# Kernel optimization log

Measured on AMD Instinct MI355X. Metric: run time of the kernel, lower is better.

The kernel has to match this reference:

```python
import jax, jax.numpy as jnp
import numpy as np

B, S, CS, H, G, P, N = 2, 4096, 256, 32, 1, 64, 128
NC = S // CS  # number of chunks


def setup_inputs() -> dict:
    key = jax.random.key(0)
    ks = jax.random.split(key, 7)
    cb = jax.random.normal(ks[0], (B, NC, G, CS, CS), jnp.float32) * 0.1
    x = jax.random.normal(ks[1], (B, S, H, P), jnp.float32)
    dt = jax.random.uniform(ks[2], (B, H, NC, CS), jnp.float32, 0.0, 0.1)
    # dA_cumsum is a (negative) cumulative log-decay within each chunk
    dA_cumsum = -jnp.cumsum(jax.random.uniform(ks[3], (B, H, NC, CS), jnp.float32, 0.0, 0.05), axis=-1)
    C = jax.random.normal(ks[4], (B, S, G, N), jnp.float32) * 0.1
    prev_states = jax.random.normal(ks[5], (B, NC, H, P, N), jnp.float32) * 0.1
    D = jax.random.normal(ks[6], (H,), jnp.float32)
    return {"cb": cb, "x": x, "dt": dt, "dA_cumsum": dA_cumsum, "C": C,
            "prev_states": prev_states, "D": D}


def reference(cb, x, dt, dA_cumsum, C, prev_states, D):
    # Reshape sequence into chunks
    x_c = x.reshape(B, NC, CS, H, P)          # b c l h p
    C_c = C.reshape(B, NC, CS, G, N)          # b c l g n
    rep = H // G
    # expand groups to heads
    C_h = jnp.repeat(C_c, rep, axis=3)        # b c l h n
    cb_h = jnp.repeat(cb, rep, axis=2)        # b c h m k

    # --- inter-chunk contribution: (C @ prev_states^T) * exp(dA_cs_m) ---
    out_inter = jnp.einsum('bclhn,bchpn->bclhp', C_h, prev_states)
    scale_m = jnp.exp(dA_cumsum)              # b h c l
    out_inter = out_inter * scale_m.transpose(0, 2, 3, 1)[..., None]

    # --- intra-chunk causal contribution ---
    # decay[m,k] = exp(dA_m - dA_k), masked to m >= k, weighted by dt_k
    dA = dA_cumsum                            # b h c l
    decay = jnp.exp(dA[..., :, None] - dA[..., None, :])  # b h c m k
    causal = jnp.tril(jnp.ones((CS, CS), jnp.bool_))
    scores = jnp.where(causal, cb_h.transpose(0, 2, 1, 3, 4) * decay * dt[..., None, :], 0.0)  # b h c m k
    out_intra = jnp.einsum('bhcmk,bckhp->bcmhp', scores, x_c)

    out = out_inter + out_intra + x_c * D[None, None, None, :, None]
    return out.reshape(B, S, H, P)
```

## Files before the change

kernel.cpp:

```cpp
#include <hip/hip_runtime.h>


typedef unsigned short u16;
typedef __bf16 v8bf __attribute__((ext_vector_type(8)));
typedef unsigned short v8u16 __attribute__((ext_vector_type(8)));
typedef float v4f __attribute__((ext_vector_type(4)));

#define LDB 264

__device__ __forceinline__ unsigned pk2f(float a, float b) {
  u16 x = __builtin_bit_cast(u16, (__bf16)a);
  u16 y = __builtin_bit_cast(u16, (__bf16)b);
  return (unsigned)x | ((unsigned)y << 16);
}
__device__ __forceinline__ v8bf cvt8(float4 lo, float4 hi) {
  v8bf r;
  r[0] = (__bf16)lo.x; r[1] = (__bf16)lo.y; r[2] = (__bf16)lo.z; r[3] = (__bf16)lo.w;
  r[4] = (__bf16)hi.x; r[5] = (__bf16)hi.y; r[6] = (__bf16)hi.z; r[7] = (__bf16)hi.w;
  return r;
}
__device__ __forceinline__ v8bf cvt8_mask(float4 lo, float4 hi, int k0, int m) {
  const float av[8] = {lo.x, lo.y, lo.z, lo.w, hi.x, hi.y, hi.z, hi.w};
  v8bf r;
#pragma unroll
  for (int j = 0; j < 8; j++) r[j] = (__bf16)((k0 + j <= m) ? av[j] : 0.f);
  return r;
}

__global__ __launch_bounds__(512, 4) void mamba_cs_kernel(
    const float* __restrict__ cbp,
    const float* __restrict__ xp,
    const float* __restrict__ dtp,
    const float* __restrict__ dAp,
    const float* __restrict__ Cp,
    const float* __restrict__ pvp,
    const float* __restrict__ Dp,
    float* __restrict__ outp)
{
  __shared__ u16 sB[64 * LDB];

  const int bid0 = blockIdx.x;
  const int wg = ((bid0 & 7) << 7) | (bid0 >> 3);
  const int h = wg & 31;
  const int c = (wg >> 5) & 15;
  const int b = wg >> 9;
  const int t = threadIdx.x;
  const int lane = t & 63;
  const int wid = t >> 6;
  const int row = lane & 15;
  const int q = lane >> 4;
  const int qo = q * 8;

  const int Ta = wid;
  const int Tb = 15 - wid;
  const int ma = Ta * 16 + row;
  const int mb = Tb * 16 + row;

  const int base_hc = ((b * 32 + h) * 16 + c) * 256;
  const float Dh = Dp[h];

  const float* CBbase = cbp + (size_t)(b * 16 + c) * 65536;
  const float* Cbase  = Cp + (size_t)(b * 4096 + c * 256) * 128;
  const float* Pbase  = pvp + (size_t)((b * 16 + c) * 32 + h) * 8192;
  const float* Xbase  = xp + ((size_t)(b * 4096 + c * 256) * 32 + h) * 64;

  v4f acc[2][4];
  float4 dAq[2];

#pragma unroll
  for (int tt = 0; tt < 2; ++tt) {
    const int T = tt ? Tb : Ta;
    const int m4 = T * 16 + q * 4;
    const float4 dA4 = *(const float4*)(dAp + base_hc + m4);
    const float4 dt4 = *(const float4*)(dtp + base_hc + m4);
    dAq[tt] = dA4;
    float xv[4][4];
#pragma unroll
    for (int r = 0; r < 4; ++r) {
      const float* xr = Xbase + (size_t)(m4 + r) * 2048 + row;
#pragma unroll
      for (int pt = 0; pt < 4; ++pt) xv[r][pt] = xr[pt * 16];
    }
    const float dv[4] = {dA4.x, dA4.y, dA4.z, dA4.w};
    const float tv[4] = {dt4.x, dt4.y, dt4.z, dt4.w};
    float wi[4], w[4];
#pragma unroll
    for (int r = 0; r < 4; ++r) {
      wi[r] = __expf(-dv[r]);
      w[r] = wi[r] * tv[r];
    }
#pragma unroll
    for (int pt = 0; pt < 4; ++pt) {
      v4f a;
#pragma unroll
      for (int r = 0; r < 4; ++r) a[r] = Dh * xv[r][pt] * wi[r];
      acc[tt][pt] = a;
      u16* srow = &sB[(pt * 16 + row) * LDB + m4];
      *(unsigned*)(srow)     = pk2f(w[0] * xv[0][pt], w[1] * xv[1][pt]);
      *(unsigned*)(srow + 2) = pk2f(w[2] * xv[2][pt], w[3] * xv[3][pt]);
    }
  }

  {
    const float* Cra = Cbase + (size_t)ma * 128;
    const float* Crb = Cbase + (size_t)mb * 128;
#pragma unroll
    for (int kf = 0; kf < 4; ++kf) {
      const int no = kf * 32 + qo;
      v8bf bf[4];
#pragma unroll
      for (int pt = 0; pt < 4; ++pt) {
        const float* pr = Pbase + (size_t)(pt * 16 + row) * 128 + no;
        bf[pt] = cvt8(*(const float4*)pr, *(const float4*)(pr + 4));
      }
      const v8bf a0 = cvt8(*(const float4*)(Cra + no), *(const float4*)(Cra + no + 4));
      const v8bf a1 = cvt8(*(const float4*)(Crb + no), *(const float4*)(Crb + no + 4));
#pragma unroll
      for (int pt = 0; pt < 4; ++pt) {
        acc[0][pt] = __builtin_amdgcn_mfma_f32_16x16x32_bf16(a0, bf[pt], acc[0][pt], 0, 0, 0);
        acc[1][pt] = __builtin_amdgcn_mfma_f32_16x16x32_bf16(a1, bf[pt], acc[1][pt], 0, 0, 0);
      }
    }
  }

  __syncthreads();

  {
    const float* cba = CBbase + (size_t)ma * 256;
    const float* cbb = CBbase + (size_t)mb * 256;
    const int kfa = Ta >> 1;
    const int kfb = Tb >> 1;
    float4 alo = *(const float4*)(cba + qo);
    float4 ahi = *(const float4*)(cba + qo + 4);
    float4 blo = *(const float4*)(cbb + qo);
    float4 bhi = *(const float4*)(cbb + qo + 4);
    for (int kf = 0; kf <= kfb; ++kf) {
      const int ko = kf * 32 + qo;
      float4 nalo = alo, nahi = ahi, nblo = blo, nbhi = bhi;
      if (kf < kfb) {
        const int nko = ko + 32;
        nblo = *(const float4*)(cbb + nko);
        nbhi = *(const float4*)(cbb + nko + 4);
        if (kf + 1 <= kfa) {
          nalo = *(const float4*)(cba + nko);
          nahi = *(const float4*)(cba + nko + 4);
        }
      }
      v8bf bf[4];
#pragma unroll
      for (int pt = 0; pt < 4; ++pt)
        bf[pt] = __builtin_bit_cast(v8bf, *(const v8u16*)&sB[(pt * 16 + row) * LDB + ko]);
      {
        const v8bf ab = (kf == kfb) ? cvt8_mask(blo, bhi, ko, mb) : cvt8(blo, bhi);
#pragma unroll
        for (int pt = 0; pt < 4; ++pt)
          acc[1][pt] = __builtin_amdgcn_mfma_f32_16x16x32_bf16(ab, bf[pt], acc[1][pt], 0, 0, 0);
      }
      if (kf <= kfa) {
        const v8bf aa = (kf == kfa) ? cvt8_mask(alo, ahi, ko, ma) : cvt8(alo, ahi);
#pragma unroll
        for (int pt = 0; pt < 4; ++pt)
          acc[0][pt] = __builtin_amdgcn_mfma_f32_16x16x32_bf16(aa, bf[pt], acc[0][pt], 0, 0, 0);
      }
      alo = nalo; ahi = nahi; blo = nblo; bhi = nbhi;
    }
  }

  float* Obase = outp + ((size_t)(b * 4096 + c * 256) * 32 + h) * 64;
  const int Ts[2] = {Ta, Tb};
#pragma unroll
  for (int tt = 0; tt < 2; ++tt) {
    const int mBase = Ts[tt] * 16 + q * 4;
    const float ev[4] = {dAq[tt].x, dAq[tt].y, dAq[tt].z, dAq[tt].w};
#pragma unroll
    for (int r = 0; r < 4; ++r) {
      const float e = __expf(ev[r]);
      float* orow = Obase + (size_t)(mBase + r) * 2048 + row;
#pragma unroll
      for (int pt = 0; pt < 4; ++pt) orow[pt * 16] = acc[tt][pt][r] * e;
    }
  }
}

extern "C" void kernel_launch(void* const* d_in, const int* in_sizes, int n_in,
                              void* d_out, int out_size, void* d_ws, size_t ws_size,
                              hipStream_t stream) {
  const float* cb = (const float*)d_in[0];
  const float* x = (const float*)d_in[1];
  const float* dt = (const float*)d_in[2];
  const float* dA = (const float*)d_in[3];
  const float* C = (const float*)d_in[4];
  const float* pv = (const float*)d_in[5];
  const float* D = (const float*)d_in[6];
  float* out = (float*)d_out;
  mamba_cs_kernel<<<dim3(1024), dim3(512), 0, stream>>>(cb, x, dt, dA, C, pv, D, out);
}
```

Before: 213.4 us.

## Stage prev_states through LDS as bf16 and prefetch C/CB loads

Loads the per-head prev_states tile once cooperatively with coalesced float4 reads, converts it to bf16 and stores it in a new shared buffer. Previously each wave re-read it from global memory with strided per-lane loads. All x/dA/dt loads are issued before any compute, and the C and CB first fragments are prefetched before the barrier, with C software-pipelined across the inter-chunk MFMA loop. The cost is extra LDS (about 17KB more per block) and more live registers, which may reduce occupancy under the 512x4 launch bounds.

```diff
diff --git a/kernel.cpp b/kernel.cpp
--- a/kernel.cpp
+++ b/kernel.cpp
@@ -7,6 +7,7 @@
 typedef float v4f __attribute__((ext_vector_type(4)));
 
 #define LDB 264
+#define LDP 136
 
 __device__ __forceinline__ unsigned pk2f(float a, float b) {
   u16 x = __builtin_bit_cast(u16, (__bf16)a);
@@ -38,6 +39,7 @@
     float* __restrict__ outp)
 {
   __shared__ u16 sB[64 * LDB];
+  __shared__ u16 sP[64 * LDP];
 
   const int bid0 = blockIdx.x;
   const int wg = ((bid0 & 7) << 7) | (bid0 >> 3);
@@ -64,76 +66,111 @@
   const float* Pbase  = pvp + (size_t)((b * 16 + c) * 32 + h) * 8192;
   const float* Xbase  = xp + ((size_t)(b * 4096 + c * 256) * 32 + h) * 64;
 
+  float4 pf[4];
+  {
+    const float4* Pv = (const float4*)Pbase;
+#pragma unroll
+    for (int i = 0; i < 4; i++) pf[i] = Pv[i * 512 + t];
+  }
+
   v4f acc[2][4];
   float4 dAq[2];
 
-#pragma unroll
-  for (int tt = 0; tt < 2; ++tt) {
-    const int T = tt ? Tb : Ta;
-    const int m4 = T * 16 + q * 4;
-    const float4 dA4 = *(const float4*)(dAp + base_hc + m4);
-    const float4 dt4 = *(const float4*)(dtp + base_hc + m4);
-    dAq[tt] = dA4;
-    float xv[4][4];
-#pragma unroll
-    for (int r = 0; r < 4; ++r) {
-      const float* xr = Xbase + (size_t)(m4 + r) * 2048 + row;
-#pragma unroll
-      for (int pt = 0; pt < 4; ++pt) xv[r][pt] = xr[pt * 16];
-    }
-    const float dv[4] = {dA4.x, dA4.y, dA4.z, dA4.w};
-    const float tv[4] = {dt4.x, dt4.y, dt4.z, dt4.w};
-    float wi[4], w[4];
-#pragma unroll
-    for (int r = 0; r < 4; ++r) {
-      wi[r] = __expf(-dv[r]);
-      w[r] = wi[r] * tv[r];
-    }
+  {
+    float4 dA4[2], dt4[2];
+    float xv[2][4][4];
+#pragma unroll
+    for (int tt = 0; tt < 2; ++tt) {
+      const int T = tt ? Tb : Ta;
+      const int m4 = T * 16 + q * 4;
+      dA4[tt] = *(const float4*)(dAp + base_hc + m4);
+      dt4[tt] = *(const float4*)(dtp + base_hc + m4);
+#pragma unroll
+      for (int r = 0; r < 4; ++r) {
+        const float* xr = Xbase + (size_t)(m4 + r) * 2048 + row;
+#pragma unroll
+        for (int pt = 0; pt < 4; ++pt) xv[tt][r][pt] = xr[pt * 16];
+      }
+    }
+#pragma unroll
+    for (int tt = 0; tt < 2; ++tt) {
+      const int T = tt ? Tb : Ta;
+      const int m4 = T * 16 + q * 4;
+      dAq[tt] = dA4[tt];
+      const float dv[4] = {dA4[tt].x, dA4[tt].y, dA4[tt].z, dA4[tt].w};
+      const float tv[4] = {dt4[tt].x, dt4[tt].y, dt4[tt].z, dt4[tt].w};
+      float wi[4], w[4];
+#pragma unroll
+      for (int r = 0; r < 4; ++r) {
+        wi[r] = __expf(-dv[r]);
+        w[r] = wi[r] * tv[r];
+      }
+#pragma unroll
+      for (int pt = 0; pt < 4; ++pt) {
+        v4f a;
+#pragma unroll
+        for (int r = 0; r < 4; ++r) a[r] = Dh * xv[tt][r][pt] * wi[r];
+        acc[tt][pt] = a;
+        u16* srow = &sB[(pt * 16 + row) * LDB + m4];
+        *(unsigned*)(srow)     = pk2f(w[0] * xv[tt][0][pt], w[1] * xv[tt][1][pt]);
+        *(unsigned*)(srow + 2) = pk2f(w[2] * xv[tt][2][pt], w[3] * xv[tt][3][pt]);
+      }
+    }
+  }
+
+#pragma unroll
+  for (int i = 0; i < 4; i++) {
+    const int idx = i * 512 + t;
+    const int prow = idx >> 5;
+    const int c4 = idx & 31;
+    u16* s = &sP[prow * LDP + c4 * 4];
+    *(unsigned*)(s)     = pk2f(pf[i].x, pf[i].y);
+    *(unsigned*)(s + 2) = pk2f(pf[i].z, pf[i].w);
+  }
+
+  const float* Cra = Cbase + (size_t)ma * 128;
+  const float* Crb = Cbase + (size_t)mb * 128;
+  const float* cba = CBbase + (size_t)ma * 256;
+  const float* cbb = CBbase + (size_t)mb * 256;
+  float4 ca0 = *(const float4*)(Cra + qo);
+  float4 ca1 = *(const float4*)(Cra + qo + 4);
+  float4 cc0 = *(const float4*)(Crb + qo);
+  float4 cc1 = *(const float4*)(Crb + qo + 4);
+  float4 alo = *(const float4*)(cba + qo);
+  float4 ahi = *(const float4*)(cba + qo + 4);
+  float4 blo = *(const float4*)(cbb + qo);
+  float4 bhi = *(const float4*)(cbb + qo + 4);
+
+  __syncthreads();
+
+#pragma unroll
+  for (int kf = 0; kf < 4; ++kf) {
+    const int no = kf * 32 + qo;
+    float4 nca0 = ca0, nca1 = ca1, ncc0 = cc0, ncc1 = cc1;
+    if (kf < 3) {
+      const int nn = no + 32;
+      nca0 = *(const float4*)(Cra + nn);
+      nca1 = *(const float4*)(Cra + nn + 4);
+      ncc0 = *(const float4*)(Crb + nn);
+      ncc1 = *(const float4*)(Crb + nn + 4);
+    }
+    v8bf bf[4];
+#pragma unroll
+    for (int pt = 0; pt < 4; ++pt)
+      bf[pt] = __builtin_bit_cast(v8bf, *(const v8u16*)&sP[(pt * 16 + row) * LDP + no]);
+    const v8bf a0 = cvt8(ca0, ca1);
+    const v8bf a1 = cvt8(cc0, cc1);
 #pragma unroll
     for (int pt = 0; pt < 4; ++pt) {
-      v4f a;
-#pragma unroll
-      for (int r = 0; r < 4; ++r) a[r] = Dh * xv[r][pt] * wi[r];
-      acc[tt][pt] = a;
-      u16* srow = &sB[(pt * 16 + row) * LDB + m4];
-      *(unsigned*)(srow)     = pk2f(w[0] * xv[0][pt], w[1] * xv[1][pt]);
-      *(unsigned*)(srow + 2) = pk2f(w[2] * xv[2][pt], w[3] * xv[3][pt]);
-    }
+      acc[0][pt] = __builtin_amdgcn_mfma_f32_16x16x32_bf16(a0, bf[pt], acc[0][pt], 0, 0, 0);
+      acc[1][pt] = __builtin_amdgcn_mfma_f32_16x16x32_bf16(a1, bf[pt], acc[1][pt], 0, 0, 0);
+    }
+    ca0 = nca0; ca1 = nca1; cc0 = ncc0; cc1 = ncc1;
   }
 
   {
-    const float* Cra = Cbase + (size_t)ma * 128;
-    const float* Crb = Cbase + (size_t)mb * 128;
-#pragma unroll
-    for (int kf = 0; kf < 4; ++kf) {
-      const int no = kf * 32 + qo;
-      v8bf bf[4];
-#pragma unroll
-      for (int pt = 0; pt < 4; ++pt) {
-        const float* pr = Pbase + (size_t)(pt * 16 + row) * 128 + no;
-        bf[pt] = cvt8(*(const float4*)pr, *(const float4*)(pr + 4));
-      }
-      const v8bf a0 = cvt8(*(const float4*)(Cra + no), *(const float4*)(Cra + no + 4));
-      const v8bf a1 = cvt8(*(const float4*)(Crb + no), *(const float4*)(Crb + no + 4));
-#pragma unroll
-      for (int pt = 0; pt < 4; ++pt) {
-        acc[0][pt] = __builtin_amdgcn_mfma_f32_16x16x32_bf16(a0, bf[pt], acc[0][pt], 0, 0, 0);
-        acc[1][pt] = __builtin_amdgcn_mfma_f32_16x16x32_bf16(a1, bf[pt], acc[1][pt], 0, 0, 0);
-      }
-    }
-  }
-
-  __syncthreads();
-
-  {
-    const float* cba = CBbase + (size_t)ma * 256;
-    const float* cbb = CBbase + (size_t)mb * 256;
     const int kfa = Ta >> 1;
     const int kfb = Tb >> 1;
-    float4 alo = *(const float4*)(cba + qo);
-    float4 ahi = *(const float4*)(cba + qo + 4);
-    float4 blo = *(const float4*)(cbb + qo);
-    float4 bhi = *(const float4*)(cbb + qo + 4);
     for (int kf = 0; kf <= kfb; ++kf) {
       const int ko = kf * 32 + qo;
       float4 nalo = alo, nahi = ahi, nblo = blo, nbhi = bhi;
```

Result: faster. 197.2 us (-7.6%).

## Process four heads per block, reusing C and CB fragments with register-prefetched stages

Applied to the files above, without the earlier changes.

Each block now handles four heads of one (batch, chunk) instead of one head, so the C and masked CB operand fragments are loaded and converted to bf16 once and kept in registers across heads. prev_states is staged through a new shared-memory tile, and the next head's x, dt, dA and prev_states are prefetched into registers while the current head's MFMAs run. This is meant to cut redundant global traffic on cb and C and hide load latency. In exchange the grid drops from 1024 to 256 blocks, which may underfill the GPU, and the higher register use lowers the occupancy bound.

```diff
diff --git a/kernel.cpp b/kernel.cpp
--- a/kernel.cpp
+++ b/kernel.cpp
@@ -7,6 +7,7 @@
 typedef float v4f __attribute__((ext_vector_type(4)));
 
 #define LDB 264
+#define LDP 136
 
 __device__ __forceinline__ unsigned pk2f(float a, float b) {
   u16 x = __builtin_bit_cast(u16, (__bf16)a);
@@ -27,7 +28,13 @@
   return r;
 }
 
-__global__ __launch_bounds__(512, 4) void mamba_cs_kernel(
+struct SR {
+  float4 pf[4];
+  float4 dA4[2], dt4[2];
+  float xv[2][4][4];
+};
+
+__global__ __launch_bounds__(512, 2) void mamba_cs_kernel(
     const float* __restrict__ cbp,
     const float* __restrict__ xp,
     const float* __restrict__ dtp,
@@ -38,12 +45,15 @@
     float* __restrict__ outp)
 {
   __shared__ u16 sB[64 * LDB];
+  __shared__ u16 sP[64 * LDP];
 
   const int bid0 = blockIdx.x;
-  const int wg = ((bid0 & 7) << 7) | (bid0 >> 3);
-  const int h = wg & 31;
-  const int c = (wg >> 5) & 15;
-  const int b = wg >> 9;
+  const int wg = ((bid0 & 7) << 5) | (bid0 >> 3);
+  const int hg = wg & 7;
+  const int c = (wg >> 3) & 15;
+  const int b = wg >> 7;
+  const int h0 = hg * 4;
+
   const int t = threadIdx.x;
   const int lane = t & 63;
   const int wid = t >> 6;
@@ -55,131 +65,178 @@
   const int Tb = 15 - wid;
   const int ma = Ta * 16 + row;
   const int mb = Tb * 16 + row;
-
-  const int base_hc = ((b * 32 + h) * 16 + c) * 256;
-  const float Dh = Dp[h];
+  const int kfa = Ta >> 1;
+  const int kfb = Tb >> 1;
 
   const float* CBbase = cbp + (size_t)(b * 16 + c) * 65536;
   const float* Cbase  = Cp + (size_t)(b * 4096 + c * 256) * 128;
-  const float* Pbase  = pvp + (size_t)((b * 16 + c) * 32 + h) * 8192;
-  const float* Xbase  = xp + ((size_t)(b * 4096 + c * 256) * 32 + h) * 64;
+
+  const float* Cra = Cbase + (size_t)ma * 128;
+  const float* Crb = Cbase + (size_t)mb * 128;
+  const float* cba = CBbase + (size_t)ma * 256;
+  const float* cbb = CBbase + (size_t)mb * 256;
+
+  v8bf Ca[4], Cb2[4];
+  v8bf Aa[4], Ab[8];
+#pragma unroll
+  for (int kf = 0; kf < 4; ++kf) {
+    const int no = kf * 32 + qo;
+    Ca[kf]  = cvt8(*(const float4*)(Cra + no), *(const float4*)(Cra + no + 4));
+    Cb2[kf] = cvt8(*(const float4*)(Crb + no), *(const float4*)(Crb + no + 4));
+  }
+#pragma unroll
+  for (int kf = 0; kf < 4; ++kf)
+    if (kf <= kfa) {
+      const int ko = kf * 32 + qo;
+      const float4 lo = *(const float4*)(cba + ko);
+      const float4 hi = *(const float4*)(cba + ko + 4);
+      Aa[kf] = (kf == kfa) ? cvt8_mask(lo, hi, ko, ma) : cvt8(lo, hi);
+    }
+#pragma unroll
+  for (int kf = 0; kf < 8; ++kf)
+    if (kf <= kfb) {
+      const int ko = kf * 32 + qo;
+      const float4 lo = *(const float4*)(cbb + ko);
+      const float4 hi = *(const float4*)(cbb + ko + 4);
+      Ab[kf] = (kf == kfb) ? cvt8_mask(lo, hi, ko, mb) : cvt8(lo, hi);
+    }
 
   v4f acc[2][4];
   float4 dAq[2];
 
-#pragma unroll
-  for (int tt = 0; tt < 2; ++tt) {
-    const int T = tt ? Tb : Ta;
-    const int m4 = T * 16 + q * 4;
-    const float4 dA4 = *(const float4*)(dAp + base_hc + m4);
-    const float4 dt4 = *(const float4*)(dtp + base_hc + m4);
-    dAq[tt] = dA4;
-    float xv[4][4];
-#pragma unroll
-    for (int r = 0; r < 4; ++r) {
-      const float* xr = Xbase + (size_t)(m4 + r) * 2048 + row;
-#pragma unroll
-      for (int pt = 0; pt < 4; ++pt) xv[r][pt] = xr[pt * 16];
-    }
-    const float dv[4] = {dA4.x, dA4.y, dA4.z, dA4.w};
-    const float tv[4] = {dt4.x, dt4.y, dt4.z, dt4.w};
-    float wi[4], w[4];
-#pragma unroll
-    for (int r = 0; r < 4; ++r) {
-      wi[r] = __expf(-dv[r]);
-      w[r] = wi[r] * tv[r];
-    }
-#pragma unroll
-    for (int pt = 0; pt < 4; ++pt) {
-      v4f a;
-#pragma unroll
-      for (int r = 0; r < 4; ++r) a[r] = Dh * xv[r][pt] * wi[r];
-      acc[tt][pt] = a;
-      u16* srow = &sB[(pt * 16 + row) * LDB + m4];
-      *(unsigned*)(srow)     = pk2f(w[0] * xv[0][pt], w[1] * xv[1][pt]);
-      *(unsigned*)(srow + 2) = pk2f(w[2] * xv[2][pt], w[3] * xv[3][pt]);
-    }
-  }
-
-  {
-    const float* Cra = Cbase + (size_t)ma * 128;
-    const float* Crb = Cbase + (size_t)mb * 128;
+  auto stage_load = [&](int h, SR& R) {
+    const float4* Pv = (const float4*)(pvp + (size_t)((b * 16 + c) * 32 + h) * 8192);
+#pragma unroll
+    for (int i = 0; i < 4; i++) R.pf[i] = Pv[i * 512 + t];
+    const int bhc = ((b * 32 + h) * 16 + c) * 256;
+    const float* Xb = xp + ((size_t)(b * 4096 + c * 256) * 32 + h) * 64;
+#pragma unroll
+    for (int tt = 0; tt < 2; ++tt) {
+      const int m4 = (tt ? Tb : Ta) * 16 + q * 4;
+      R.dA4[tt] = *(const float4*)(dAp + bhc + m4);
+      R.dt4[tt] = *(const float4*)(dtp + bhc + m4);
+#pragma unroll
+      for (int r = 0; r < 4; ++r) {
+        const float* xr = Xb + (size_t)(m4 + r) * 2048 + row;
+#pragma unroll
+        for (int pt = 0; pt < 4; ++pt) R.xv[tt][r][pt] = xr[pt * 16];
+      }
+    }
+  };
+
+  auto commit = [&](SR& R, float Dh) {
+#pragma unroll
+    for (int i = 0; i < 4; i++) {
+      const int idx = i * 512 + t, prow = idx >> 5, c4 = idx & 31;
+      u16* s = &sP[prow * LDP + c4 * 4];
+      *(unsigned*)(s)     = pk2f(R.pf[i].x, R.pf[i].y);
+      *(unsigned*)(s + 2) = pk2f(R.pf[i].z, R.pf[i].w);
+    }
+#pragma unroll
+    for (int tt = 0; tt < 2; ++tt) {
+      const int m4 = (tt ? Tb : Ta) * 16 + q * 4;
+      dAq[tt] = R.dA4[tt];
+      const float dv[4] = {R.dA4[tt].x, R.dA4[tt].y, R.dA4[tt].z, R.dA4[tt].w};
+      const float tv[4] = {R.dt4[tt].x, R.dt4[tt].y, R.dt4[tt].z, R.dt4[tt].w};
+      float wi[4], w[4];
+#pragma unroll
+      for (int r = 0; r < 4; ++r) {
+        wi[r] = __expf(-dv[r]);
+        w[r] = wi[r] * tv[r];
+      }
+#pragma unroll
+      for (int pt = 0; pt < 4; ++pt) {
+        v4f a;
+#pragma unroll
+        for (int r = 0; r < 4; ++r) a[r] = Dh * R.xv[tt][r][pt] * wi[r];
+        acc[tt][pt] = a;
+        u16* srow = &sB[(pt * 16 + row) * LDB + m4];
+        *(unsigned*)(srow)     = pk2f(w[0] * R.xv[tt][0][pt], w[1] * R.xv[tt][1][pt]);
+        *(unsigned*)(srow + 2) = pk2f(w[2] * R.xv[tt][2][pt], w[3] * R.xv[tt][3][pt]);
+      }
+    }
+  };
+
+  auto compute = [&]() {
 #pragma unroll
     for (int kf = 0; kf < 4; ++kf) {
       const int no = kf * 32 + qo;
       v8bf bf[4];
 #pragma unroll
+      for (int pt = 0; pt < 4; ++pt)
+        bf[pt] = __builtin_bit_cast(v8bf, *(const v8u16*)&sP[(pt * 16 + row) * LDP + no]);
+#pragma unroll
       for (int pt = 0; pt < 4; ++pt) {
-        const float* pr = Pbase + (size_t)(pt * 16 + row) * 128 + no;
-        bf[pt] = cvt8(*(const float4*)pr, *(const float4*)(pr + 4));
-      }
-      const v8bf a0 = cvt8(*(const float4*)(Cra + no), *(const float4*)(Cra + no + 4));
-      const v8bf a1 = cvt8(*(const float4*)(Crb + no), *(const float4*)(Crb + no + 4));
-#pragma unroll
-      for (int pt = 0; pt < 4; ++pt) {
-        acc[0][pt] = __builtin_amdgcn_mfma_f32_16x16x32_bf16(a0, bf[pt], acc[0][pt], 0, 0, 0);
-        acc[1][pt] = __builtin_amdgcn_mfma_f32_16x16x32_bf16(a1, bf[pt], acc[1][pt], 0, 0, 0);
-      }
-    }
-  }
-
-  __syncthreads();
-
-  {
-    const float* cba = CBbase + (size_t)ma * 256;
-    const float* cbb = CBbase + (size_t)mb * 256;
-    const int kfa = Ta >> 1;
-    const int kfb = Tb >> 1;
-    float4 alo = *(const float4*)(cba + qo);
-    float4 ahi = *(const float4*)(cba + qo + 4);
-    float4 blo = *(const float4*)(cbb + qo);
-    float4 bhi = *(const float4*)(cbb + qo + 4);
-    for (int kf = 0; kf <= kfb; ++kf) {
-      const int ko = kf * 32 + qo;
-      float4 nalo = alo, nahi = ahi, nblo = blo, nbhi = bhi;
-      if (kf < kfb) {
-        const int nko = ko + 32;
-        nblo = *(const float4*)(cbb + nko);
-        nbhi = *(const float4*)(cbb + nko + 4);
-        if (kf + 1 <= kfa) {
-          nalo = *(const float4*)(cba + nko);
-          nahi = *(const float4*)(cba + nko + 4);
+        acc[0][pt] = __builtin_amdgcn_mfma_f32_16x16x32_bf16(Ca[kf], bf[pt], acc[0][pt], 0, 0, 0);
+        acc[1][pt] = __builtin_amdgcn_mfma_f32_16x16x32_bf16(Cb2[kf], bf[pt], acc[1][pt], 0, 0, 0);
+      }
+    }
+#pragma unroll
+    for (int kf = 0; kf < 8; ++kf) {
+      if (kf <= kfb) {
+        const int ko = kf * 32 + qo;
+        v8bf bf[4];
+#pragma unroll
+        for (int pt = 0; pt < 4; ++pt)
+          bf[pt] = __builtin_bit_cast(v8bf, *(const v8u16*)&sB[(pt * 16 + row) * LDB + ko]);
+#pragma unroll
+        for (int pt = 0; pt < 4; ++pt)
+          acc[1][pt] = __builtin_amdgcn_mfma_f32_16x16x32_bf16(Ab[kf], bf[pt], acc[1][pt], 0, 0, 0);
+        if (kf <= kfa) {
+#pragma unroll
+          for (int pt = 0; pt < 4; ++pt)
+            acc[0][pt] = __builtin_amdgcn_mfma_f32_16x16x32_bf16(Aa[kf], bf[pt], acc[0][pt], 0, 0, 0);
         }
       }
-      v8bf bf[4];
-#pragma unroll
-      for (int pt = 0; pt < 4; ++pt)
-        bf[pt] = __builtin_bit_cast(v8bf, *(const v8u16*)&sB[(pt * 16 + row) * LDB + ko]);
-      {
-        const v8bf ab = (kf == kfb) ? cvt8_mask(blo, bhi, ko, mb) : cvt8(blo, bhi);
-#pragma unroll
-        for (int pt = 0; pt < 4; ++pt)
-          acc[1][pt] = __builtin_amdgcn_mfma_f32_16x16x32_bf16(ab, bf[pt], acc[1][pt], 0, 0, 0);
-      }
-      if (kf <= kfa) {
-        const v8bf aa = (kf == kfa) ? cvt8_mask(alo, ahi, ko, ma) : cvt8(alo, ahi);
-#pragma unroll
-        for (int pt = 0; pt < 4; ++pt)
-          acc[0][pt] = __builtin_amdgcn_mfma_f32_16x16x32_bf16(aa, bf[pt], acc[0][pt], 0, 0, 0);
-      }
-      alo = nalo; ahi = nahi; blo = nblo; bhi = nbhi;
-    }
-  }
-
-  float* Obase = outp + ((size_t)(b * 4096 + c * 256) * 32 + h) * 64;
-  const int Ts[2] = {Ta, Tb};
-#pragma unroll
-  for (int tt = 0; tt < 2; ++tt) {
-    const int mBase = Ts[tt] * 16 + q * 4;
-    const float ev[4] = {dAq[tt].x, dAq[tt].y, dAq[tt].z, dAq[tt].w};
-#pragma unroll
-    for (int r = 0; r < 4; ++r) {
-      const float e = __expf(ev[r]);
-      float* orow = Obase + (size_t)(mBase + r) * 2048 + row;
-#pragma unroll
-      for (int pt = 0; pt < 4; ++pt) orow[pt * 16] = acc[tt][pt][r] * e;
-    }
-  }
+    }
+  };
+
+  auto epilogue = [&](int h) {
+    float* Ob = outp + ((size_t)(b * 4096 + c * 256) * 32 + h) * 64;
+#pragma unroll
+    for (int tt = 0; tt < 2; ++tt) {
+      const int mBase = (tt ? Tb : Ta) * 16 + q * 4;
+      const float ev[4] = {dAq[tt].x, dAq[tt].y, dAq[tt].z, dAq[tt].w};
+#pragma unroll
+      for (int r = 0; r < 4; ++r) {
+        const float e = __expf(ev[r]);
+        float* orow = Ob + (size_t)(mBase + r) * 2048 + row;
+#pragma unroll
+        for (int pt = 0; pt < 4; ++pt) orow[pt * 16] = acc[tt][pt][r] * e;
+      }
+    }
+  };
+
+  const float D0 = Dp[h0], D1 = Dp[h0 + 1], D2 = Dp[h0 + 2], D3 = Dp[h0 + 3];
+
+  SR RA, RB;
+  stage_load(h0, RA);
+
+  commit(RA, D0);
+  __syncthreads();
+  stage_load(h0 + 1, RB);
+  compute();
+  epilogue(h0);
+  __syncthreads();
+
+  commit(RB, D1);
+  __syncthreads();
+  stage_load(h0 + 2, RA);
+  compute();
+  epilogue(h0 + 1);
+  __syncthreads();
+
+  commit(RA, D2);
+  __syncthreads();
+  stage_load(h0 + 3, RB);
+  compute();
+  epilogue(h0 + 2);
+  __syncthreads();
+
+  commit(RB, D3);
+  __syncthreads();
+  compute();
+  epilogue(h0 + 3);
 }
 
 extern "C" void kernel_launch(void* const* d_in, const int* in_sizes, int n_in,
@@ -193,5 +250,5 @@
   const float* pv = (const float*)d_in[5];
   const float* D = (const float*)d_in[6];
   float* out = (float*)d_out;
-  mamba_cs_kernel<<<dim3(1024), dim3(512), 0, stream>>>(cb, x, dt, dA, C, pv, D, out);
-}
+  mamba_cs_kernel<<<dim3(256), dim3(512), 0, stream>>>(cb, x, dt, dA, C, pv, D, out);
+}
```

Result: faster. 176.4 us (-17.4%).

## Process four heads per block with staged prev_states in LDS and prefetch

Applied to the files above, without the earlier changes.

Each block now covers four consecutive heads of one (batch, chunk) with 1024 threads, one 16-row tile per wave, instead of one head with 512 threads and paired tiles. The C operand is converted to bf16 once and kept in registers for all four heads. The next head's prev_states, x, dt and dA are prefetched while the current head computes, and prev_states is staged into LDS as bf16 instead of being read per lane from global. The grid shrinks to 256 blocks, which cuts parallelism, and the per-wave causal work is now uneven across waves instead of being balanced by tile pairing.

```diff
diff --git a/kernel.cpp b/kernel.cpp
--- a/kernel.cpp
+++ b/kernel.cpp
@@ -5,8 +5,10 @@
 typedef __bf16 v8bf __attribute__((ext_vector_type(8)));
 typedef unsigned short v8u16 __attribute__((ext_vector_type(8)));
 typedef float v4f __attribute__((ext_vector_type(4)));
+typedef unsigned v2u __attribute__((ext_vector_type(2)));
 
 #define LDB 264
+#define LDP 136
 
 __device__ __forceinline__ unsigned pk2f(float a, float b) {
   u16 x = __builtin_bit_cast(u16, (__bf16)a);
@@ -27,7 +29,7 @@
   return r;
 }
 
-__global__ __launch_bounds__(512, 4) void mamba_cs_kernel(
+__global__ __launch_bounds__(1024, 4) void mamba_cs_kernel(
     const float* __restrict__ cbp,
     const float* __restrict__ xp,
     const float* __restrict__ dtp,
@@ -38,12 +40,15 @@
     float* __restrict__ outp)
 {
   __shared__ u16 sB[64 * LDB];
+  __shared__ u16 sP[64 * LDP];
 
   const int bid0 = blockIdx.x;
-  const int wg = ((bid0 & 7) << 7) | (bid0 >> 3);
-  const int h = wg & 31;
-  const int c = (wg >> 5) & 15;
-  const int b = wg >> 9;
+  const int wg = ((bid0 & 7) << 5) | (bid0 >> 3);
+  const int hg = wg & 7;
+  const int c = (wg >> 3) & 15;
+  const int b = wg >> 7;
+  const int h0 = hg * 4;
+
   const int t = threadIdx.x;
   const int lane = t & 63;
   const int wid = t >> 6;
@@ -51,36 +56,57 @@
   const int q = lane >> 4;
   const int qo = q * 8;
 
-  const int Ta = wid;
-  const int Tb = 15 - wid;
-  const int ma = Ta * 16 + row;
-  const int mb = Tb * 16 + row;
-
-  const int base_hc = ((b * 32 + h) * 16 + c) * 256;
-  const float Dh = Dp[h];
+  const int T = wid;
+  const int ma = T * 16 + row;
+  const int m4 = T * 16 + q * 4;
+  const int kfa = T >> 1;
 
   const float* CBbase = cbp + (size_t)(b * 16 + c) * 65536;
-  const float* Cbase  = Cp + (size_t)(b * 4096 + c * 256) * 128;
-  const float* Pbase  = pvp + (size_t)((b * 16 + c) * 32 + h) * 8192;
-  const float* Xbase  = xp + ((size_t)(b * 4096 + c * 256) * 32 + h) * 64;
+  const float* cba = CBbase + (size_t)ma * 256;
+  const float* Cra = Cp + (size_t)(b * 4096 + c * 256) * 128 + (size_t)ma * 128;
 
-  v4f acc[2][4];
-  float4 dAq[2];
+  v8bf Ca[4];
+#pragma unroll
+  for (int kf = 0; kf < 4; ++kf) {
+    const int no = kf * 32 + qo;
+    Ca[kf] = cvt8(*(const float4*)(Cra + no), *(const float4*)(Cra + no + 4));
+  }
 
-#pragma unroll
-  for (int tt = 0; tt < 2; ++tt) {
-    const int T = tt ? Tb : Ta;
-    const int m4 = T * 16 + q * 4;
-    const float4 dA4 = *(const float4*)(dAp + base_hc + m4);
-    const float4 dt4 = *(const float4*)(dtp + base_hc + m4);
-    dAq[tt] = dA4;
-    float xv[4][4];
+  const float4 Dv = *(const float4*)(Dp + h0);
+  const float Dhs[4] = {Dv.x, Dv.y, Dv.z, Dv.w};
+
+  float4 pf0, pf1, dA4, dt4;
+  float xv[4][4];
+  v4f acc[4];
+  float4 dAq;
+
+  auto stage_load = [&](int h) {
+    const float4* Pv = (const float4*)(pvp + (size_t)((b * 16 + c) * 32 + h) * 8192);
+    pf0 = Pv[t];
+    pf1 = Pv[1024 + t];
+    const int bhc = ((b * 32 + h) * 16 + c) * 256;
+    dA4 = *(const float4*)(dAp + bhc + m4);
+    dt4 = *(const float4*)(dtp + bhc + m4);
+    const float* Xb = xp + ((size_t)(b * 4096 + c * 256) * 32 + h) * 64;
 #pragma unroll
     for (int r = 0; r < 4; ++r) {
-      const float* xr = Xbase + (size_t)(m4 + r) * 2048 + row;
+      const float* xr = Xb + (size_t)(m4 + r) * 2048 + row;
 #pragma unroll
       for (int pt = 0; pt < 4; ++pt) xv[r][pt] = xr[pt * 16];
     }
+  };
+
+  auto commit = [&](float Dh) {
+#pragma unroll
+    for (int j = 0; j < 2; ++j) {
+      const int idx = j * 1024 + t, prow = idx >> 5, c4 = idx & 31;
+      const float4 p4 = j ? pf1 : pf0;
+      v2u wv;
+      wv[0] = pk2f(p4.x, p4.y);
+      wv[1] = pk2f(p4.z, p4.w);
+      *(v2u*)&sP[prow * LDP + c4 * 4] = wv;
+    }
+    dAq = dA4;
     const float dv[4] = {dA4.x, dA4.y, dA4.z, dA4.w};
     const float tv[4] = {dt4.x, dt4.y, dt4.z, dt4.w};
     float wi[4], w[4];
@@ -94,91 +120,64 @@
       v4f a;
 #pragma unroll
       for (int r = 0; r < 4; ++r) a[r] = Dh * xv[r][pt] * wi[r];
-      acc[tt][pt] = a;
-      u16* srow = &sB[(pt * 16 + row) * LDB + m4];
-      *(unsigned*)(srow)     = pk2f(w[0] * xv[0][pt], w[1] * xv[1][pt]);
-      *(unsigned*)(srow + 2) = pk2f(w[2] * xv[2][pt], w[3] * xv[3][pt]);
+      acc[pt] = a;
+      v2u wv;
+      wv[0] = pk2f(w[0] * xv[0][pt], w[1] * xv[1][pt]);
+      wv[1] = pk2f(w[2] * xv[2][pt], w[3] * xv[3][pt]);
+      *(v2u*)&sB[(pt * 16 + row) * LDB + m4] = wv;
     }
-  }
+  };
 
-  {
-    const float* Cra = Cbase + (size_t)ma * 128;
-    const float* Crb = Cbase + (size_t)mb * 128;
+  auto compute = [&]() {
 #pragma unroll
     for (int kf = 0; kf < 4; ++kf) {
       const int no = kf * 32 + qo;
       v8bf bf[4];
 #pragma unroll
-      for (int pt = 0; pt < 4; ++pt) {
-        const float* pr = Pbase + (size_t)(pt * 16 + row) * 128 + no;
-        bf[pt] = cvt8(*(const float4*)pr, *(const float4*)(pr + 4));
-      }
-      const v8bf a0 = cvt8(*(const float4*)(Cra + no), *(const float4*)(Cra + no + 4));
-      const v8bf a1 = cvt8(*(const float4*)(Crb + no), *(const float4*)(Crb + no + 4));
+      for (int pt = 0; pt < 4; ++pt)
+        bf[pt] = __builtin_bit_cast(v8bf, *(const v8u16*)&sP[(pt * 16 + row) * LDP + no]);
 #pragma unroll
-      for (int pt = 0; pt < 4; ++pt) {
-        acc[0][pt] = __builtin_amdgcn_mfma_f32_16x16x32_bf16(a0, bf[pt], acc[0][pt], 0, 0, 0);
-        acc[1][pt] = __builtin_amdgcn_mfma_f32_16x16x32_bf16(a1, bf[pt], acc[1][pt], 0, 0, 0);
+      for (int pt = 0; pt < 4; ++pt)
+        acc[pt] = __builtin_amdgcn_mfma_f32_16x16x32_bf16(Ca[kf], bf[pt], acc[pt], 0, 0, 0);
+    }
+#pragma unroll
+    for (int kf = 0; kf < 8; ++kf) {
+      if (kf <= kfa) {
+        const int ko = kf * 32 + qo;
+        const float4 lo = *(const float4*)(cba + ko);
+        const float4 hi = *(const float4*)(cba + ko + 4);
+        v8bf bf[4];
+#pragma unroll
+        for (int pt = 0; pt < 4; ++pt)
+          bf[pt] = __builtin_bit_cast(v8bf, *(const v8u16*)&sB[(pt * 16 + row) * LDB + ko]);
+        const v8bf a = (kf == kfa) ? cvt8_mask(lo, hi, ko, ma) : cvt8(lo, hi);
+#pragma unroll
+        for (int pt = 0; pt < 4; ++pt)
+          acc[pt] = __builtin_amdgcn_mfma_f32_16x16x32_bf16(a, bf[pt], acc[pt], 0, 0, 0);
       }
     }
-  }
+  };
 
-  __syncthreads();
-
-  {
-    const float* cba = CBbase + (size_t)ma * 256;
-    const float* cbb = CBbase + (size_t)mb * 256;
-    const int kfa = Ta >> 1;
-    const int kfb = Tb >> 1;
-    float4 alo = *(const float4*)(cba + qo);
-    float4 ahi = *(const float4*)(cba + qo + 4);
-    float4 blo = *(const float4*)(cbb + qo);
-    float4 bhi = *(const float4*)(cbb + qo + 4);
-    for (int kf = 0; kf <= kfb; ++kf) {
-      const int ko = kf * 32 + qo;
-      float4 nalo = alo, nahi = ahi, nblo = blo, nbhi = bhi;
-      if (kf < kfb) {
-        const int nko = ko + 32;
-        nblo = *(const float4*)(cbb + nko);
-        nbhi = *(const float4*)(cbb + nko + 4);
-        if (kf + 1 <= kfa) {
-          nalo = *(const float4*)(cba + nko);
-          nahi = *(const float4*)(cba + nko + 4);
-        }
-      }
-      v8bf bf[4];
-#pragma unroll
-      for (int pt = 0; pt < 4; ++pt)
-        bf[pt] = __builtin_bit_cast(v8bf, *(const v8u16*)&sB[(pt * 16 + row) * LDB + ko]);
-      {
-        const v8bf ab = (kf == kfb) ? cvt8_mask(blo, bhi, ko, mb) : cvt8(blo, bhi);
-#pragma unroll
-        for (int pt = 0; pt < 4; ++pt)
-          acc[1][pt] = __builtin_amdgcn_mfma_f32_16x16x32_bf16(ab, bf[pt], acc[1][pt], 0, 0, 0);
-      }
-      if (kf <= kfa) {
-        const v8bf aa = (kf == kfa) ? cvt8_mask(alo, ahi, ko, ma) : cvt8(alo, ahi);
-#pragma unroll
-        for (int pt = 0; pt < 4; ++pt)
-          acc[0][pt] = __builtin_amdgcn_mfma_f32_16x16x32_bf16(aa, bf[pt], acc[0][pt], 0, 0, 0);
-      }
-      alo = nalo; ahi = nahi; blo = nblo; bhi = nbhi;
-    }
-  }
-
-  float* Obase = outp + ((size_t)(b * 4096 + c * 256) * 32 + h) * 64;
-  const int Ts[2] = {Ta, Tb};
-#pragma unroll
-  for (int tt = 0; tt < 2; ++tt) {
-    const int mBase = Ts[tt] * 16 + q * 4;
-    const float ev[4] = {dAq[tt].x, dAq[tt].y, dAq[tt].z, dAq[tt].w};
+  auto epilogue = [&](int h) {
+    float* Ob = outp + ((size_t)(b * 4096 + c * 256) * 32 + h) * 64;
+    const float ev[4] = {dAq.x, dAq.y, dAq.z, dAq.w};
 #pragma unroll
     for (int r = 0; r < 4; ++r) {
       const float e = __expf(ev[r]);
-      float* orow = Obase + (size_t)(mBase + r) * 2048 + row;
+      float* orow = Ob + (size_t)(m4 + r) * 2048 + row;
 #pragma unroll
-      for (int pt = 0; pt < 4; ++pt) orow[pt * 16] = acc[tt][pt][r] * e;
+      for (int pt = 0; pt < 4; ++pt) orow[pt * 16] = acc[pt][r] * e;
     }
+  };
+
+  stage_load(h0);
+  for (int hh = 0; hh < 4; ++hh) {
+    commit(Dhs[hh]);
+    __syncthreads();
+    if (hh < 3) stage_load(h0 + hh + 1);
+    compute();
+    epilogue(h0 + hh);
+    if (hh < 3) __syncthreads();
   }
 }
 
@@ -193,5 +192,5 @@
   const float* pv = (const float*)d_in[5];
   const float* D = (const float*)d_in[6];
   float* out = (float*)d_out;
-  mamba_cs_kernel<<<dim3(1024), dim3(512), 0, stream>>>(cb, x, dt, dA, C, pv, D, out);
+  mamba_cs_kernel<<<dim3(256), dim3(1024), 0, stream>>>(cb, x, dt, dA, C, pv, D, out);
 }
```

Measured after the change: 181.7 us. 1.17x faster.
